# Optimization experiments

Hardware: AMD Instinct MI355X
Metric: run time of the kernel (lower is better)

The kernel has to match this reference:

```python
import jax, jax.numpy as jnp
import numpy as np

IN_DIM = 512
POS_RFACTOR = 8
MAX_POS = 128
WP = MAX_POS // POS_RFACTOR  # pooled 1D width = 16


def _sin_table(max_len, d):
    # HANet-style sinusoidal table; row 0 is all zeros
    pos = np.arange(max_len)[:, None].astype(np.float64)
    j = np.arange(d)[None, :]
    angle = pos / np.power(10000.0, 2 * (j // 2) / d)
    enc = np.zeros((max_len, d), dtype=np.float32)
    enc[1:, 0::2] = np.sin(angle[1:, 0::2])
    enc[1:, 1::2] = np.cos(angle[1:, 1::2])
    return jnp.asarray(enc)


def setup_inputs() -> dict:
    key = jax.random.key(0)
    ks = jax.random.split(key, 6)
    B, C, H, W = 4, IN_DIM, 64, 64
    Ck = C // 2
    s = 1.0 / np.sqrt(C)
    return {
        "x": jax.random.normal(ks[0], (B, C, H, W), jnp.float32),
        "Wq": jax.random.normal(ks[1], (Ck, C), jnp.float32) * s,
        "bq": jnp.zeros((Ck,), jnp.float32),
        "Wk": jax.random.normal(ks[2], (Ck, C), jnp.float32) * s,
        "bk": jnp.zeros((Ck,), jnp.float32),
        "Wv": jax.random.normal(ks[3], (C, C), jnp.float32) * s,
        "bv": jnp.zeros((C,), jnp.float32),
        "gamma": jnp.ones((1,), jnp.float32),  # torch inits to 0; nonzero here so output/grads are non-trivial
        "pe_table": _sin_table(MAX_POS, C),
        "pos": jax.random.randint(ks[4], (B, H, W), 0, MAX_POS, dtype=jnp.int32),
    }


def reference(x, Wq, bq, Wk, bk, Wv, bv, gamma, pe_table, pos):
    B, C, H, W = x.shape
    # colpool: AdaptiveAvgPool2d((1, WP)) -> mean over H, block-mean over W (W % WP == 0)
    x1d = x.mean(axis=2).reshape(B, C, WP, W // WP).mean(axis=-1)  # B,C,WP
    # PosEncoding1D (eval mode, no noise): select first row, //rfactor, nearest-resize to WP, embed
    p = pos[:, 0, :] // POS_RFACTOR                 # B,W
    nidx = (jnp.arange(WP) * W) // WP               # nearest-neighbor indices
    pe = pe_table[p[:, nidx]]                       # B,WP,C
    x1d = x1d + jnp.transpose(pe, (0, 2, 1))        # B,C,WP
    # Upsample(x1d.unsqueeze(2), (H,W)): bilinear align_corners=True; height dim is 1 -> constant
    src = jnp.arange(W, dtype=jnp.float32) * (WP - 1) / (W - 1)
    i0 = jnp.floor(src).astype(jnp.int32)
    i1 = jnp.minimum(i0 + 1, WP - 1)
    t = (src - i0.astype(jnp.float32)).astype(x.dtype)
    row = x1d[:, :, i0] * (1.0 - t) + x1d[:, :, i1] * t  # B,C,W
    x2d = jnp.broadcast_to(row[:, :, None, :], (B, C, H, W))
    # 1x1 conv projections
    q = jnp.einsum('bchw,oc->bohw', x, Wq) + bq[None, :, None, None]
    k = jnp.einsum('bchw,oc->bohw', x2d, Wk) + bk[None, :, None, None]
    v = jnp.einsum('bchw,oc->bohw', x, Wv) + bv[None, :, None, None]
    N = H * W
    q = q.reshape(B, -1, N)   # B,Ck,N
    k = k.reshape(B, -1, N)   # B,Ck,N
    v = v.reshape(B, C, N)    # B,C,N
    energy = jnp.einsum('bcn,bcm->bnm', q, k)        # B,N,N (query n, key m), unscaled
    attn = jax.nn.softmax(energy, axis=-1)
    out = jnp.einsum('bcm,bnm->bcn', v, attn)        # B,C,N
    out = out.reshape(B, C, H, W)
    return gamma[0] * out + x
```

## Files before the change

### kernel.cpp

```cpp
#include <hip/hip_runtime.h>

#define CDIM 512
#define OKD  256
#define NDIM 4096

#define OFF_XMH 0
#define OFF_X1  131072
#define OFF_K1  163840
#define OFF_M1A 180224
#define OFF_CB1 196608
#define OFF_VMB 196672

typedef float f32x4  __attribute__((ext_vector_type(4)));
typedef short shortx4 __attribute__((ext_vector_type(4)));
typedef short shortx8 __attribute__((ext_vector_type(8)));

static __device__ __forceinline__ unsigned short f2bf(float f) {
  unsigned u = __float_as_uint(f);
  u = (u + 0x7FFFu + ((u >> 16) & 1u)) >> 16;
  return (unsigned short)u;
}
static __device__ __forceinline__ unsigned pk2(float lo, float hi) {
  return (unsigned)f2bf(lo) | ((unsigned)f2bf(hi) << 16);
}

__global__ __launch_bounds__(256) void k_reduce(const float* __restrict__ x,
                                                const float* __restrict__ pe,
                                                const int* __restrict__ pos,
                                                float* __restrict__ xmh,
                                                float* __restrict__ x1pe) {
  int t = threadIdx.x;
  int bc = blockIdx.x * 4 + (t >> 6);
  int w4 = t & 15;
  int hoff = (t >> 4) & 3;
  const float4* xp = (const float4*)(x) + (size_t)bc * (64 * 16);
  float4 acc = make_float4(0.f, 0.f, 0.f, 0.f);
#pragma unroll
  for (int k = 0; k < 16; ++k) {
    float4 v = xp[(hoff + 4 * k) * 16 + w4];
    acc.x += v.x; acc.y += v.y; acc.z += v.z; acc.w += v.w;
  }
  acc.x += __shfl_xor(acc.x, 16); acc.y += __shfl_xor(acc.y, 16);
  acc.z += __shfl_xor(acc.z, 16); acc.w += __shfl_xor(acc.w, 16);
  acc.x += __shfl_xor(acc.x, 32); acc.y += __shfl_xor(acc.y, 32);
  acc.z += __shfl_xor(acc.z, 32); acc.w += __shfl_xor(acc.w, 32);
  if (hoff == 0) {
    const float inv = 1.f / 64.f;
    float4 o = make_float4(acc.x * inv, acc.y * inv, acc.z * inv, acc.w * inv);
    ((float4*)xmh)[bc * 16 + w4] = o;
    int b = bc >> 9;
    int c = bc & 511;
    int ps = pos[b * 4096 + 4 * w4] >> 3;
    float x1 = (o.x + o.y + o.z + o.w) * 0.25f + pe[ps * CDIM + c];
    x1pe[bc * 16 + w4] = x1;
  }
}

__global__ __launch_bounds__(128) void k_vmk1(const float* __restrict__ Wv,
                                              const float* __restrict__ bv,
                                              const float* __restrict__ Wk,
                                              const float* __restrict__ bk,
                                              const float* __restrict__ xmh,
                                              const float* __restrict__ x1pe,
                                              unsigned short* __restrict__ vmb,
                                              float* __restrict__ K1) {
  int t = threadIdx.x;
  int blk = blockIdx.x;
  if (blk < 64) {
    int wid = blk * 2 + (t >> 6);
    int lane = t & 63, nrel = lane & 15, kg = lane >> 4;
    int b = wid >> 5, rem = wid & 31, cgrp = rem >> 2, wt = rem & 3;
    f32x4 acc[4] = {{0,0,0,0},{0,0,0,0},{0,0,0,0},{0,0,0,0}};
    for (int kt = 0; kt < 16; ++kt) {
      const float* xp = xmh + (size_t)(b * 512 + kt * 32 + kg * 4) * 64 + wt * 16 + nrel;
      float v0 = xp[0], v1 = xp[64], v2 = xp[128], v3 = xp[192];
      float v4 = xp[1024], v5 = xp[1088], v6 = xp[1152], v7 = xp[1216];
      shortx8 bf;
      unsigned* bu = (unsigned*)&bf;
      bu[0] = pk2(v0, v1); bu[1] = pk2(v2, v3);
      bu[2] = pk2(v4, v5); bu[3] = pk2(v6, v7);
#pragma unroll
      for (int m = 0; m < 4; ++m) {
        int c = (cgrp * 4 + m) * 16 + nrel;
        const float* wp = Wv + (size_t)c * 512 + kt * 32 + kg * 4;
        float4 a0 = *(const float4*)wp;
        float4 a1 = *(const float4*)(wp + 16);
        shortx8 af;
        unsigned* au = (unsigned*)&af;
        au[0] = pk2(a0.x, a0.y); au[1] = pk2(a0.z, a0.w);
        au[2] = pk2(a1.x, a1.y); au[3] = pk2(a1.z, a1.w);
        acc[m] = __builtin_amdgcn_mfma_f32_16x16x32_bf16(af, bf, acc[m], 0, 0, 0);
      }
    }
#pragma unroll
    for (int m = 0; m < 4; ++m)
#pragma unroll
      for (int r = 0; r < 4; ++r) {
        int c = (cgrp * 4 + m) * 16 + kg * 4 + r;
        vmb[(size_t)(b * 512 + c) * 64 + wt * 16 + nrel] = f2bf(acc[m][r] + bv[c]);
      }
  } else {
    int idx = blk - 64;
    int b = idx >> 5, og = idx & 31;
    int o = og * 8 + (t >> 4), i = t & 15;
    const float* Wr = Wk + (size_t)o * 512;
    const float* xb = x1pe + ((size_t)b * 512) * 16 + i;
    float a0 = 0.f, a1 = 0.f, a2 = 0.f, a3 = 0.f;
    for (int c = 0; c < 512; c += 4) {
      a0 += Wr[c]     * xb[c * 16];
      a1 += Wr[c + 1] * xb[(c + 1) * 16];
      a2 += Wr[c + 2] * xb[(c + 2) * 16];
      a3 += Wr[c + 3] * xb[(c + 3) * 16];
    }
    K1[((b << 8) + o) * 16 + i] = bk[o] + a0 + a1 + a2 + a3;
  }
}

__global__ __launch_bounds__(256) void k_m1(const float* __restrict__ Wq,
                                            const float* __restrict__ bq,
                                            const float* __restrict__ K1,
                                            unsigned short* __restrict__ m1A,
                                            float* __restrict__ cb1) {
  int t = threadIdx.x;
  int blk = blockIdx.x;
  if (blk < 32) {
    int lane = t & 63, nrel = lane & 15, kg = lane >> 4;
    int job = blk * 4 + (t >> 6);
    int b = job >> 5, ct = job & 31;
    f32x4 acc = {0.f, 0.f, 0.f, 0.f};
#pragma unroll
    for (int kt = 0; kt < 8; ++kt) {
      const float* wqp = Wq + (size_t)(kt * 32 + kg * 4) * CDIM + ct * 16 + nrel;
      float a0 = wqp[0],          a1 = wqp[CDIM],      a2 = wqp[2 * CDIM],  a3 = wqp[3 * CDIM];
      float a4 = wqp[16 * CDIM],  a5 = wqp[17 * CDIM], a6 = wqp[18 * CDIM], a7 = wqp[19 * CDIM];
      shortx8 af;
      unsigned* au = (unsigned*)&af;
      au[0] = pk2(a0, a1); au[1] = pk2(a2, a3);
      au[2] = pk2(a4, a5); au[3] = pk2(a6, a7);
      const float* kp = K1 + ((size_t)(b * 256 + kt * 32 + kg * 4)) * 16 + nrel;
      float b0 = kp[0],   b1 = kp[16],  b2 = kp[32],  b3 = kp[48];
      float b4 = kp[256], b5 = kp[272], b6 = kp[288], b7 = kp[304];
      shortx8 bf;
      unsigned* bu = (unsigned*)&bf;
      bu[0] = pk2(b0, b1); bu[1] = pk2(b2, b3);
      bu[2] = pk2(b4, b5); bu[3] = pk2(b6, b7);
      acc = __builtin_amdgcn_mfma_f32_16x16x32_bf16(af, bf, acc, 0, 0, 0);
    }
#pragma unroll
    for (int r = 0; r < 4; ++r) {
      int c = ct * 16 + kg * 4 + r;
      int ktm = c >> 5, klm = c & 31;
      int kgm = (klm < 16) ? (klm >> 2) : ((klm - 16) >> 2);
      int jm = (klm & 3) + ((klm < 16) ? 0 : 4);
      m1A[(size_t)b * 8192 + ((size_t)(ktm * 16 + nrel) * 4 + kgm) * 8 + jm] = f2bf(acc[r]);
    }
  } else if (t < 64) {
    int b = t >> 4, i = t & 15;
    const float* Kb = K1 + (b << 8) * 16 + i;
    float acc = 0.f;
    for (int o = 0; o < OKD; ++o) acc += bq[o] * Kb[o * 16];
    cb1[b * 16 + i] = acc;
  }
}

__global__ __launch_bounds__(512, 4) void k_attn(const float* __restrict__ x,
                                                 const unsigned short* __restrict__ m1A,
                                                 const float* __restrict__ cb1,
                                                 const unsigned short* __restrict__ vmb,
                                                 const float* __restrict__ gamma,
                                                 float* __restrict__ out) {
  __shared__ float e1w[8][32][17];
  __shared__ __align__(16) char p_t[4096];

  const int t = threadIdx.x;
  const int lane = t & 63;
  const int wv = t >> 6;
  const int b  = blockIdx.x >> 7;
  const int n0 = (blockIdx.x & 127) * 32;
  const int nrel = lane & 15;
  const int kg = lane >> 4;

  {
    f32x4 pacc[2] = {{0,0,0,0},{0,0,0,0}};
#pragma unroll
    for (int ktw = 0; ktw < 2; ++ktw) {
      int ktg = wv * 2 + ktw;
      shortx8 af = *(const shortx8*)(m1A + (size_t)b * 8192 +
                                     ((size_t)((ktg * 16 + nrel) * 4 + kg)) * 8);
#pragma unroll
      for (int nt = 0; nt < 2; ++nt) {
        const float* xp = x + (size_t)(b * 512 + wv * 64 + ktw * 32 + kg * 4) * NDIM +
                          n0 + nt * 16 + nrel;
        float v0 = xp[0],         v1 = xp[NDIM],       v2 = xp[2 * NDIM],  v3 = xp[3 * NDIM];
        float v4 = xp[16 * NDIM], v5 = xp[17 * NDIM],  v6 = xp[18 * NDIM], v7 = xp[19 * NDIM];
        shortx8 bf;
        unsigned* bu = (unsigned*)&bf;
        bu[0] = pk2(v0, v1); bu[1] = pk2(v2, v3);
        bu[2] = pk2(v4, v5); bu[3] = pk2(v6, v7);
        pacc[nt] = __builtin_amdgcn_mfma_f32_16x16x32_bf16(af, bf, pacc[nt], 0, 0, 0);
      }
    }
#pragma unroll
    for (int nt = 0; nt < 2; ++nt)
#pragma unroll
      for (int r = 0; r < 4; ++r)
        e1w[wv][nt * 16 + nrel][kg * 4 + r] = pacc[nt][r];
  }
  __syncthreads();

  {
    const int sn = t >> 4;
    const int si = t & 15;
    float ev = cb1[b * 16 + si];
#pragma unroll
    for (int g = 0; g < 8; ++g) ev += e1w[g][sn][si];
    float pv[4];
    float mx = -3.4e38f;
#pragma unroll
    for (int j = 0; j < 4; ++j) {
      int w = si * 4 + j;
      float srcf = (float)w * (15.0f / 63.0f);
      int i0 = (int)srcf;
      float tf = srcf - (float)i0;
      int i1 = i0 + 1; if (i1 > 15) i1 = 15;
      float v0 = __shfl(ev, (lane & 48) | i0);
      float v1 = __shfl(ev, (lane & 48) | i1);
      float vv = v0 * (1.0f - tf) + v1 * tf;
      pv[j] = vv;
      mx = fmaxf(mx, vv);
    }
    mx = fmaxf(mx, __shfl_xor(mx, 1));
    mx = fmaxf(mx, __shfl_xor(mx, 2));
    mx = fmaxf(mx, __shfl_xor(mx, 4));
    mx = fmaxf(mx, __shfl_xor(mx, 8));
    float s = 0.f;
#pragma unroll
    for (int j = 0; j < 4; ++j) { pv[j] = __expf(pv[j] - mx); s += pv[j]; }
    s += __shfl_xor(s, 1); s += __shfl_xor(s, 2);
    s += __shfl_xor(s, 4); s += __shfl_xor(s, 8);
    float inv = 1.0f / s;
    unsigned lo = pk2(pv[0] * inv, pv[1] * inv);
    unsigned hi = pk2(pv[2] * inv, pv[3] * inv);
    unsigned* dst = (unsigned*)(p_t + sn * 128 + ((si ^ (sn & 15)) << 3));
    dst[0] = lo; dst[1] = hi;
  }
  __syncthreads();

  {
    const float gm = gamma[0];
#pragma unroll
    for (int j = 0; j < 8; ++j) {
      const int idx = wv * 8 + j;
      const int ct = idx >> 1, nt = idx & 1;
      f32x4 dacc = {0.f, 0.f, 0.f, 0.f};
      const unsigned short* vrow =
          vmb + ((size_t)(b * CDIM + ct * 16 + nrel)) * 64 + kg * 4;
      const char* prow = p_t + (nt * 16 + nrel) * 128;
#pragma unroll
      for (int ks = 0; ks < 2; ++ks) {
        shortx4 a0 = *(const shortx4*)(vrow + ks * 32);
        shortx4 a1 = *(const shortx4*)(vrow + ks * 32 + 16);
        shortx8 av = __builtin_shufflevector(a0, a1, 0, 1, 2, 3, 4, 5, 6, 7);
        int G0 = (ks * 8 + kg) ^ nrel;
        int G1 = (ks * 8 + 4 + kg) ^ nrel;
        shortx4 b0 = *(const shortx4*)(prow + G0 * 8);
        shortx4 b1 = *(const shortx4*)(prow + G1 * 8);
        shortx8 bv2 = __builtin_shufflevector(b0, b1, 0, 1, 2, 3, 4, 5, 6, 7);
        dacc = __builtin_amdgcn_mfma_f32_16x16x32_bf16(av, bv2, dacc, 0, 0, 0);
      }
#pragma unroll
      for (int r = 0; r < 4; ++r) {
        int c_o = ct * 16 + kg * 4 + r;
        size_t base = (size_t)(b * CDIM + c_o) * NDIM + n0 + nt * 16 + nrel;
        out[base] = gm * dacc[r] + x[base];
      }
    }
  }
}

extern "C" void kernel_launch(void* const* d_in, const int* in_sizes, int n_in,
                              void* d_out, int out_size, void* d_ws, size_t ws_size,
                              hipStream_t stream) {
  const float* x     = (const float*)d_in[0];
  const float* Wq    = (const float*)d_in[1];
  const float* bq    = (const float*)d_in[2];
  const float* Wk    = (const float*)d_in[3];
  const float* bk    = (const float*)d_in[4];
  const float* Wv    = (const float*)d_in[5];
  const float* bv    = (const float*)d_in[6];
  const float* gamma = (const float*)d_in[7];
  const float* pe    = (const float*)d_in[8];
  const int*   pos   = (const int*)d_in[9];
  float* out = (float*)d_out;
  float* ws  = (float*)d_ws;

  float* xmh  = ws + OFF_XMH;
  float* x1pe = ws + OFF_X1;
  float* K1   = ws + OFF_K1;
  unsigned short* m1A = (unsigned short*)(ws + OFF_M1A);
  float* cb1  = ws + OFF_CB1;
  unsigned short* vmb = (unsigned short*)(ws + OFF_VMB);

  hipLaunchKernelGGL(k_reduce, dim3(512), dim3(256), 0, stream, x, pe, pos, xmh, x1pe);
  hipLaunchKernelGGL(k_vmk1, dim3(192), dim3(128), 0, stream, Wv, bv, Wk, bk, xmh, x1pe, vmb, K1);
  hipLaunchKernelGGL(k_m1, dim3(33), dim3(256), 0, stream, Wq, bq, K1, m1A, cb1);
  hipLaunchKernelGGL(k_attn, dim3(512), dim3(512), 0, stream, x, m1A, cb1, vmb, gamma, out);
}
```

Measured before the change: 136.4 us.

## Fuse K1 projection and M1 product into one mid kernel with MFMA

Result: slower. 195.0 us (+43.0%).

```diff
diff --git a/kernel.cpp b/kernel.cpp
--- a/kernel.cpp
+++ b/kernel.cpp
@@ -6,10 +6,9 @@
 
 #define OFF_XMH 0
 #define OFF_X1  131072
-#define OFF_K1  163840
-#define OFF_M1A 180224
-#define OFF_CB1 196608
-#define OFF_VMB 196672
+#define OFF_M1A 163840
+#define OFF_CB1 180224
+#define OFF_VMB 180288
 
 typedef float f32x4  __attribute__((ext_vector_type(4)));
 typedef short shortx4 __attribute__((ext_vector_type(4)));
@@ -56,19 +55,23 @@
   }
 }
 
-__global__ __launch_bounds__(128) void k_vmk1(const float* __restrict__ Wv,
-                                              const float* __restrict__ bv,
-                                              const float* __restrict__ Wk,
-                                              const float* __restrict__ bk,
-                                              const float* __restrict__ xmh,
-                                              const float* __restrict__ x1pe,
-                                              unsigned short* __restrict__ vmb,
-                                              float* __restrict__ K1) {
+__global__ __launch_bounds__(256) void k_mid(const float* __restrict__ Wv,
+                                             const float* __restrict__ bv,
+                                             const float* __restrict__ Wk,
+                                             const float* __restrict__ bk,
+                                             const float* __restrict__ Wq,
+                                             const float* __restrict__ bq,
+                                             const float* __restrict__ xmh,
+                                             const float* __restrict__ x1pe,
+                                             unsigned short* __restrict__ vmb,
+                                             unsigned short* __restrict__ m1A,
+                                             float* __restrict__ cb1) {
+  __shared__ float k1s[256][17];
   int t = threadIdx.x;
   int blk = blockIdx.x;
-  if (blk < 64) {
-    int wid = blk * 2 + (t >> 6);
-    int lane = t & 63, nrel = lane & 15, kg = lane >> 4;
+  int lane = t & 63, nrel = lane & 15, kg = lane >> 4;
+  if (blk < 32) {
+    int wid = blk * 4 + (t >> 6);
     int b = wid >> 5, rem = wid & 31, cgrp = rem >> 2, wt = rem & 3;
     f32x4 acc[4] = {{0,0,0,0},{0,0,0,0},{0,0,0,0},{0,0,0,0}};
     for (int kt = 0; kt < 16; ++kt) {
@@ -100,66 +103,78 @@
         vmb[(size_t)(b * 512 + c) * 64 + wt * 16 + nrel] = f2bf(acc[m][r] + bv[c]);
       }
   } else {
-    int idx = blk - 64;
-    int b = idx >> 5, og = idx & 31;
-    int o = og * 8 + (t >> 4), i = t & 15;
-    const float* Wr = Wk + (size_t)o * 512;
-    const float* xb = x1pe + ((size_t)b * 512) * 16 + i;
-    float a0 = 0.f, a1 = 0.f, a2 = 0.f, a3 = 0.f;
-    for (int c = 0; c < 512; c += 4) {
-      a0 += Wr[c]     * xb[c * 16];
-      a1 += Wr[c + 1] * xb[(c + 1) * 16];
-      a2 += Wr[c + 2] * xb[(c + 2) * 16];
-      a3 += Wr[c + 3] * xb[(c + 3) * 16];
-    }
-    K1[((b << 8) + o) * 16 + i] = bk[o] + a0 + a1 + a2 + a3;
-  }
-}
-
-__global__ __launch_bounds__(256) void k_m1(const float* __restrict__ Wq,
-                                            const float* __restrict__ bq,
-                                            const float* __restrict__ K1,
-                                            unsigned short* __restrict__ m1A,
-                                            float* __restrict__ cb1) {
-  int t = threadIdx.x;
-  int blk = blockIdx.x;
-  if (blk < 32) {
-    int lane = t & 63, nrel = lane & 15, kg = lane >> 4;
-    int job = blk * 4 + (t >> 6);
-    int b = job >> 5, ct = job & 31;
-    f32x4 acc = {0.f, 0.f, 0.f, 0.f};
-#pragma unroll
-    for (int kt = 0; kt < 8; ++kt) {
-      const float* wqp = Wq + (size_t)(kt * 32 + kg * 4) * CDIM + ct * 16 + nrel;
-      float a0 = wqp[0],          a1 = wqp[CDIM],      a2 = wqp[2 * CDIM],  a3 = wqp[3 * CDIM];
-      float a4 = wqp[16 * CDIM],  a5 = wqp[17 * CDIM], a6 = wqp[18 * CDIM], a7 = wqp[19 * CDIM];
-      shortx8 af;
-      unsigned* au = (unsigned*)&af;
-      au[0] = pk2(a0, a1); au[1] = pk2(a2, a3);
-      au[2] = pk2(a4, a5); au[3] = pk2(a6, a7);
-      const float* kp = K1 + ((size_t)(b * 256 + kt * 32 + kg * 4)) * 16 + nrel;
-      float b0 = kp[0],   b1 = kp[16],  b2 = kp[32],  b3 = kp[48];
-      float b4 = kp[256], b5 = kp[272], b6 = kp[288], b7 = kp[304];
-      shortx8 bf;
-      unsigned* bu = (unsigned*)&bf;
-      bu[0] = pk2(b0, b1); bu[1] = pk2(b2, b3);
-      bu[2] = pk2(b4, b5); bu[3] = pk2(b6, b7);
-      acc = __builtin_amdgcn_mfma_f32_16x16x32_bf16(af, bf, acc, 0, 0, 0);
-    }
-#pragma unroll
-    for (int r = 0; r < 4; ++r) {
-      int c = ct * 16 + kg * 4 + r;
-      int ktm = c >> 5, klm = c & 31;
-      int kgm = (klm < 16) ? (klm >> 2) : ((klm - 16) >> 2);
-      int jm = (klm & 3) + ((klm < 16) ? 0 : 4);
-      m1A[(size_t)b * 8192 + ((size_t)(ktm * 16 + nrel) * 4 + kgm) * 8 + jm] = f2bf(acc[r]);
-    }
-  } else if (t < 64) {
-    int b = t >> 4, i = t & 15;
-    const float* Kb = K1 + (b << 8) * 16 + i;
-    float acc = 0.f;
-    for (int o = 0; o < OKD; ++o) acc += bq[o] * Kb[o * 16];
-    cb1[b * 16 + i] = acc;
+    int b = blk - 32;
+    int wvi = t >> 6;
+#pragma unroll
+    for (int oti = 0; oti < 4; ++oti) {
+      int ot = wvi * 4 + oti;
+      f32x4 acc = {0.f, 0.f, 0.f, 0.f};
+#pragma unroll
+      for (int kt = 0; kt < 16; ++kt) {
+        int o = ot * 16 + nrel;
+        const float* wp = Wk + (size_t)o * 512 + kt * 32 + kg * 4;
+        float4 a0 = *(const float4*)wp;
+        float4 a1 = *(const float4*)(wp + 16);
+        shortx8 af;
+        unsigned* au = (unsigned*)&af;
+        au[0] = pk2(a0.x, a0.y); au[1] = pk2(a0.z, a0.w);
+        au[2] = pk2(a1.x, a1.y); au[3] = pk2(a1.z, a1.w);
+        const float* xp = x1pe + (size_t)(b * 512 + kt * 32 + kg * 4) * 16 + nrel;
+        float b0 = xp[0],   b1 = xp[16],  b2 = xp[32],  b3 = xp[48];
+        float b4 = xp[256], b5 = xp[272], b6 = xp[288], b7 = xp[304];
+        shortx8 bf;
+        unsigned* bu = (unsigned*)&bf;
+        bu[0] = pk2(b0, b1); bu[1] = pk2(b2, b3);
+        bu[2] = pk2(b4, b5); bu[3] = pk2(b6, b7);
+        acc = __builtin_amdgcn_mfma_f32_16x16x32_bf16(af, bf, acc, 0, 0, 0);
+      }
+#pragma unroll
+      for (int r = 0; r < 4; ++r) {
+        int o = ot * 16 + kg * 4 + r;
+        k1s[o][nrel] = acc[r] + bk[o];
+      }
+    }
+    __syncthreads();
+#pragma unroll
+    for (int cti = 0; cti < 8; ++cti) {
+      int ct = wvi * 8 + cti;
+      f32x4 acc = {0.f, 0.f, 0.f, 0.f};
+#pragma unroll
+      for (int kt = 0; kt < 8; ++kt) {
+        const float* wqp = Wq + (size_t)(kt * 32 + kg * 4) * CDIM + ct * 16 + nrel;
+        float a0 = wqp[0],         a1 = wqp[CDIM],      a2 = wqp[2 * CDIM],  a3 = wqp[3 * CDIM];
+        float a4 = wqp[16 * CDIM], a5 = wqp[17 * CDIM], a6 = wqp[18 * CDIM], a7 = wqp[19 * CDIM];
+        shortx8 af;
+        unsigned* au = (unsigned*)&af;
+        au[0] = pk2(a0, a1); au[1] = pk2(a2, a3);
+        au[2] = pk2(a4, a5); au[3] = pk2(a6, a7);
+        const float* kp = &k1s[kt * 32 + kg * 4][0] + nrel;
+        float b0 = kp[0],      b1 = kp[17],     b2 = kp[34],     b3 = kp[51];
+        float b4 = kp[16*17],  b5 = kp[17*17],  b6 = kp[18*17],  b7 = kp[19*17];
+        shortx8 bf;
+        unsigned* bu = (unsigned*)&bf;
+        bu[0] = pk2(b0, b1); bu[1] = pk2(b2, b3);
+        bu[2] = pk2(b4, b5); bu[3] = pk2(b6, b7);
+        acc = __builtin_amdgcn_mfma_f32_16x16x32_bf16(af, bf, acc, 0, 0, 0);
+      }
+#pragma unroll
+      for (int r = 0; r < 4; ++r) {
+        int c = ct * 16 + kg * 4 + r;
+        int ktm = c >> 5, klm = c & 31;
+        int kgm = (klm < 16) ? (klm >> 2) : ((klm - 16) >> 2);
+        int jm = (klm & 3) + ((klm < 16) ? 0 : 4);
+        m1A[(size_t)b * 8192 + ((size_t)(ktm * 16 + nrel) * 4 + kgm) * 8 + jm] = f2bf(acc[r]);
+      }
+    }
+    if (t < 64) {
+      int i = t & 15, og = t >> 4;
+      float s = 0.f;
+#pragma unroll 8
+      for (int m = 0; m < 64; ++m) s += bq[og * 64 + m] * k1s[og * 64 + m][i];
+      s += __shfl_xor(s, 16);
+      s += __shfl_xor(s, 32);
+      if (og == 0) cb1[b * 16 + i] = s;
+    }
   }
 }
 
@@ -296,13 +311,13 @@
 
   float* xmh  = ws + OFF_XMH;
   float* x1pe = ws + OFF_X1;
-  float* K1   = ws + OFF_K1;
   unsigned short* m1A = (unsigned short*)(ws + OFF_M1A);
   float* cb1  = ws + OFF_CB1;
   unsigned short* vmb = (unsigned short*)(ws + OFF_VMB);
 
   hipLaunchKernelGGL(k_reduce, dim3(512), dim3(256), 0, stream, x, pe, pos, xmh, x1pe);
-  hipLaunchKernelGGL(k_vmk1, dim3(192), dim3(128), 0, stream, Wv, bv, Wk, bk, xmh, x1pe, vmb, K1);
-  hipLaunchKernelGGL(k_m1, dim3(33), dim3(256), 0, stream, Wq, bq, K1, m1A, cb1);
-  hipLaunchKernelGGL(k_attn, dim3(512), dim3(512), 0, stream, x, m1A, cb1, vmb, gamma, out);
-}
+  hipLaunchKernelGGL(k_mid, dim3(36), dim3(256), 0, stream,
+                     Wv, bv, Wk, bk, Wq, bq, xmh, x1pe, vmb, m1A, cb1);
+  hipLaunchKernelGGL(k_attn, dim3(512), dim3(512), 0, stream,
+                     x, m1A, cb1, vmb, gamma, out);
+}
```
